# Kernel optimization log

Measured on AMD Instinct MI355X. Metric: run time of the kernel, lower is better.

## Reference

```python
import jax, jax.numpy as jnp
import numpy as np

N_NODES = 100000
N_EDGES = 3200000
BATCH = 16
HIDDEN = 64


def setup_inputs() -> dict:
    key = jax.random.key(0)
    k_mu, k_ei, k_w1, k_b1, k_w2, k_b2 = jax.random.split(key, 6)
    mu = jax.random.normal(k_mu, (BATCH, N_NODES), dtype=jnp.float32)
    edge_index = jax.random.randint(k_ei, (2, N_EDGES), 0, N_NODES, dtype=jnp.int64)
    # MLP params: Linear(1, hidden) -> GELU -> Linear(hidden, 1)
    W1 = jax.random.normal(k_w1, (1, HIDDEN), dtype=jnp.float32) * (1.0 / np.sqrt(1))
    b1 = jax.random.normal(k_b1, (HIDDEN,), dtype=jnp.float32) * 0.02
    W2 = jax.random.normal(k_w2, (HIDDEN, 1), dtype=jnp.float32) * (1.0 / np.sqrt(HIDDEN))
    b2 = jax.random.normal(k_b2, (1,), dtype=jnp.float32) * 0.02
    return {"mu": mu, "edge_index": edge_index, "W1": W1, "b1": b1, "W2": W2, "b2": b2}


def reference(mu, edge_index, W1, b1, W2, b2):
    row, col = edge_index[0], edge_index[1]
    B, N = mu.shape
    # degree of each destination node (clamped at 1)
    deg = jax.ops.segment_sum(jnp.ones_like(row, dtype=mu.dtype), row, num_segments=N)
    deg = jnp.maximum(deg, 1.0)  # [N]
    # batched message aggregation: gather source values, scatter-add to rows
    msgs = mu[:, col].T                                    # [E, B]
    agg = jax.ops.segment_sum(msgs, row, num_segments=N)   # [N, B]
    out = agg.T / deg[None, :]                             # [B, N]
    # tiny MLP applied per scalar: 1 -> hidden -> 1 with exact (erf) GELU
    h = jax.nn.gelu(out[..., None] * W1[0][None, None, :] + b1, approximate=False)  # [B, N, H]
    y = jnp.einsum('bnh,h->bn', h, W2[:, 0]) + b2[0]       # [B, N]
    return y
```

## Files before the change

### kernel.cpp

```cpp
#include <hip/hip_runtime.h>
#include <hip/hip_fp16.h>

#define N_NODES 100000
#define N_EDGES 3200000
#define BATCH   16
#define HIDDEN  64

#define NBINS   512
#define NPB     196
#define NSH     8
#define CAP_SH  1024
#define CAP_BIN 8192
#define EPB     8192
#define MAXW    16

#define PBLKS   391
#define TBLKS   196
#define LBLKS   17

#define LUT_SIZE  8192
#define LUT_LO    (-16.0f)
#define LUT_SCALE (LUT_SIZE / 32.0f)

typedef int v4i __attribute__((ext_vector_type(4)));

__global__ __launch_bounds__(512) void fused_part_prep_kernel(
    const int* __restrict__ ei, unsigned int* __restrict__ gcnt,
    unsigned int* __restrict__ packed,
    const float* __restrict__ mu, __half* __restrict__ mu_h,
    const float* __restrict__ W1, const float* __restrict__ b1,
    const float* __restrict__ W2, const float* __restrict__ b2,
    float* __restrict__ lut) {
  __shared__ int aux[NBINS];
  __shared__ int wsum[8];
  __shared__ unsigned int stag[EPB];
  __shared__ unsigned short sbin[EPB];

  int blk = blockIdx.x;
  int t = threadIdx.x;

  if (blk >= PBLKS) {
    if (blk < PBLKS + TBLKS) {
      int n = (blk - PBLKS) * 512 + t;
      if (n >= N_NODES) return;
      float4 o[4];
#pragma unroll
      for (int q = 0; q < 4; ++q) {
        o[q].x = mu[(q * 4 + 0) * N_NODES + n];
        o[q].y = mu[(q * 4 + 1) * N_NODES + n];
        o[q].z = mu[(q * 4 + 2) * N_NODES + n];
        o[q].w = mu[(q * 4 + 3) * N_NODES + n];
      }
      __half2 hh[8];
#pragma unroll
      for (int q = 0; q < 4; ++q) {
        hh[2 * q]     = __floats2half2_rn(o[q].x, o[q].y);
        hh[2 * q + 1] = __floats2half2_rn(o[q].z, o[q].w);
      }
      int4 w0 = make_int4(*(int*)&hh[0], *(int*)&hh[1], *(int*)&hh[2], *(int*)&hh[3]);
      int4 w1 = make_int4(*(int*)&hh[4], *(int*)&hh[5], *(int*)&hh[6], *(int*)&hh[7]);
      int4* dst = (int4*)(mu_h + (size_t)n * BATCH);
      dst[0] = w0;
      dst[1] = w1;
    } else {
      int i = (blk - PBLKS - TBLKS) * 512 + t;
      if (i > LUT_SIZE) return;
      float x = LUT_LO + (float)i / LUT_SCALE;
      float acc = b2[0];
      for (int h = 0; h < HIDDEN; ++h) {
        float z = fmaf(x, W1[h], b1[h]);
        float g = 0.5f * z * (1.0f + erff(z * 0.70710678118654752f));
        acc = fmaf(g, W2[h], acc);
      }
      lut[i] = acc;
    }
    return;
  }

  int base = blk * EPB;
  int nvalid = min(EPB, N_EDGES - base);
  int sh = blk & (NSH - 1);
  aux[t] = 0;
  __syncthreads();

  unsigned int pk[16];
  int bn[16];
  int rk[16];
  if (t * 16 + 16 <= nvalid) {
    const v4i* rp = (const v4i*)(ei + base + t * 16);
    const v4i* cp = (const v4i*)(ei + N_EDGES + base + t * 16);
    v4i rr[4], cc[4];
#pragma unroll
    for (int q = 0; q < 4; ++q) {
      rr[q] = rp[q];
      cc[q] = cp[q];
    }
#pragma unroll
    for (int q = 0; q < 4; ++q) {
#pragma unroll
      for (int u = 0; u < 4; ++u) {
        int k = q * 4 + u;
        int r = rr[q][u];
        int c = cc[q][u];
        int b = r / NPB;
        int rl = r - b * NPB;
        pk[k] = ((unsigned int)rl << 17) | (unsigned int)c;
        bn[k] = b;
      }
    }
#pragma unroll
    for (int k = 0; k < 16; ++k) rk[k] = atomicAdd(&aux[bn[k]], 1);
  } else {
#pragma unroll
    for (int k = 0; k < 16; ++k) {
      int e = t * 16 + k;
      if (e < nvalid) {
        int r = ei[base + e];
        int c = ei[N_EDGES + base + e];
        int b = r / NPB;
        int rl = r - b * NPB;
        pk[k] = ((unsigned int)rl << 17) | (unsigned int)c;
        bn[k] = b;
        rk[k] = atomicAdd(&aux[b], 1);
      } else {
        bn[k] = -1;
      }
    }
  }
  __syncthreads();

  int lane = t & 63;
  int wid = t >> 6;
  int v = aux[t];

  unsigned int gb = v ? atomicAdd(&gcnt[t * NSH + sh], (unsigned int)v) : 0u;

  int sv = v;
#pragma unroll
  for (int d = 1; d < 64; d <<= 1) {
    int n = __shfl_up(sv, d, 64);
    if (lane >= d) sv += n;
  }
  if (lane == 63) wsum[wid] = sv;
  __syncthreads();
  if (t < 8) {
    int s = wsum[t];
#pragma unroll
    for (int d = 1; d < 8; d <<= 1) {
      int n = __shfl_up(s, d, 8);
      if (t >= d) s += n;
    }
    wsum[t] = s;
  }
  __syncthreads();
  int pexcl = sv + (wid ? wsum[wid - 1] : 0) - v;
  aux[t] = pexcl;
  __syncthreads();

#pragma unroll
  for (int k = 0; k < 16; ++k) {
    if (bn[k] >= 0) {
      int p = aux[bn[k]] + rk[k];
      stag[p] = pk[k];
      sbin[p] = (unsigned short)bn[k];
    }
  }
  __syncthreads();

  aux[t] = (int)(sh * CAP_SH + gb) - pexcl;
  __syncthreads();

  unsigned int lim = (unsigned int)((sh + 1) * CAP_SH);
  for (int i = t; i < nvalid; i += 512) {
    int b = sbin[i];
    unsigned int pos = (unsigned int)(i + aux[b]);
    if (pos < lim)
      packed[(size_t)b * CAP_BIN + pos] = stag[i];
  }
}

__global__ __launch_bounds__(512) void scatter_apply_kernel(
    const unsigned int* __restrict__ gcnt, const unsigned int* __restrict__ packed,
    const __half* __restrict__ mu_h, const float* __restrict__ lut,
    float* __restrict__ out) {
  __shared__ unsigned int scol[CAP_BIN];
  __shared__ int dcnt[NPB];
  __shared__ int ebase[NPB];
  __shared__ int wpart[4];
  __shared__ int scnt_s[NSH];

  int t = threadIdx.x;
  int bin = blockIdx.x;

  const unsigned int* pp = packed + (size_t)bin * CAP_BIN;

  if (t < NPB) dcnt[t] = 0;
  if (t < NSH) scnt_s[t] = min((int)gcnt[bin * NSH + t], CAP_SH);
  __syncthreads();

  unsigned int w[MAXW];
  {
    const uint4* pp4 = (const uint4*)pp;
#pragma unroll
    for (int q = 0; q < 4; ++q) {
      uint4 a = pp4[t * 4 + q];
      w[q * 4 + 0] = a.x;
      w[q * 4 + 1] = a.y;
      w[q * 4 + 2] = a.z;
      w[q * 4 + 3] = a.w;
    }
  }

  int rk[MAXW];
#pragma unroll
  for (int k = 0; k < MAXW; ++k) {
    int i = t * 16 + k;
    int off = i & (CAP_SH - 1);
    rk[k] = (off < scnt_s[i >> 10]) ? atomicAdd(&dcnt[w[k] >> 17], 1) : 0;
  }
  __syncthreads();

  int v = 0, sv = 0;
  if (t < 256) {
    v = (t < NPB) ? dcnt[t] : 0;
    int lane = t & 63;
    sv = v;
#pragma unroll
    for (int d = 1; d < 64; d <<= 1) {
      int n = __shfl_up(sv, d, 64);
      if (lane >= d) sv += n;
    }
    if (lane == 63) wpart[t >> 6] = sv;
  }
  __syncthreads();
  if (t < 256) {
    int wid = t >> 6;
    int off = 0;
#pragma unroll
    for (int q = 0; q < 3; ++q)
      if (wid > q) off += wpart[q];
    if (t < NPB) ebase[t] = sv + off - v;
  }
  __syncthreads();

#pragma unroll
  for (int k = 0; k < MAXW; ++k) {
    int i = t * 16 + k;
    int off = i & (CAP_SH - 1);
    if (off < scnt_s[i >> 10]) {
      int rl = (int)(w[k] >> 17);
      scol[ebase[rl] + rk[k]] = w[k] & 0x1FFFFu;
    }
  }
  __syncthreads();

  const __half2* mu2 = (const __half2*)mu_h;
  int j2 = t & 7;
  int nsl = t >> 3;
  int binBase = bin * NPB;

#pragma unroll
  for (int pass = 0; pass < 4; ++pass) {
    int nl = pass * 64 + nsl;
    if (nl < NPB) {
      int node = binBase + nl;
      if (node < N_NODES) {
        int s = ebase[nl];
        int e = s + dcnt[nl];
        float2 a0 = {0.f, 0.f}, a1 = {0.f, 0.f};
        float2 a2 = {0.f, 0.f}, a3 = {0.f, 0.f};
        int i = s;
        for (; i + 8 <= e; i += 8) {
          int c0 = (int)scol[i];
          int c1 = (int)scol[i + 1];
          int c2 = (int)scol[i + 2];
          int c3 = (int)scol[i + 3];
          int c4 = (int)scol[i + 4];
          int c5 = (int)scol[i + 5];
          int c6 = (int)scol[i + 6];
          int c7 = (int)scol[i + 7];
          __half2 v0 = mu2[(size_t)c0 * 8 + j2];
          __half2 v1 = mu2[(size_t)c1 * 8 + j2];
          __half2 v2 = mu2[(size_t)c2 * 8 + j2];
          __half2 v3 = mu2[(size_t)c3 * 8 + j2];
          __half2 v4 = mu2[(size_t)c4 * 8 + j2];
          __half2 v5 = mu2[(size_t)c5 * 8 + j2];
          __half2 v6 = mu2[(size_t)c6 * 8 + j2];
          __half2 v7 = mu2[(size_t)c7 * 8 + j2];
          float2 f0 = __half22float2(v0);
          float2 f1 = __half22float2(v1);
          float2 f2 = __half22float2(v2);
          float2 f3 = __half22float2(v3);
          float2 f4 = __half22float2(v4);
          float2 f5 = __half22float2(v5);
          float2 f6 = __half22float2(v6);
          float2 f7 = __half22float2(v7);
          a0.x += f0.x + f4.x; a0.y += f0.y + f4.y;
          a1.x += f1.x + f5.x; a1.y += f1.y + f5.y;
          a2.x += f2.x + f6.x; a2.y += f2.y + f6.y;
          a3.x += f3.x + f7.x; a3.y += f3.y + f7.y;
        }
        for (; i + 4 <= e; i += 4) {
          int c0 = (int)scol[i];
          int c1 = (int)scol[i + 1];
          int c2 = (int)scol[i + 2];
          int c3 = (int)scol[i + 3];
          __half2 v0 = mu2[(size_t)c0 * 8 + j2];
          __half2 v1 = mu2[(size_t)c1 * 8 + j2];
          __half2 v2 = mu2[(size_t)c2 * 8 + j2];
          __half2 v3 = mu2[(size_t)c3 * 8 + j2];
          float2 f0 = __half22float2(v0);
          float2 f1 = __half22float2(v1);
          float2 f2 = __half22float2(v2);
          float2 f3 = __half22float2(v3);
          a0.x += f0.x; a0.y += f0.y;
          a1.x += f1.x; a1.y += f1.y;
          a2.x += f2.x; a2.y += f2.y;
          a3.x += f3.x; a3.y += f3.y;
        }
        for (; i < e; ++i) {
          float2 f = __half22float2(mu2[(size_t)scol[i] * 8 + j2]);
          a0.x += f.x; a0.y += f.y;
        }
        float sx = (a0.x + a1.x) + (a2.x + a3.x);
        float sy = (a0.y + a1.y) + (a2.y + a3.y);
        float dinv = 1.0f / (float)max(e - s, 1);

        float xs[2] = {sx * dinv, sy * dinv};
#pragma unroll
        for (int q = 0; q < 2; ++q) {
          float u = (xs[q] - LUT_LO) * LUT_SCALE;
          u = fminf(fmaxf(u, 0.0f), (float)LUT_SIZE - 0.001f);
          int ii = (int)u;
          float frac = u - (float)ii;
          float lo = lut[ii];
          float hi = lut[ii + 1];
          __builtin_nontemporal_store(fmaf(hi - lo, frac, lo),
                                      &out[(size_t)(2 * j2 + q) * N_NODES + node]);
        }
      }
    }
  }
}

extern "C" void kernel_launch(void* const* d_in, const int* in_sizes, int n_in,
                              void* d_out, int out_size, void* d_ws, size_t ws_size,
                              hipStream_t stream) {
  const float* mu = (const float*)d_in[0];
  const int*   ei = (const int*)d_in[1];
  const float* W1 = (const float*)d_in[2];
  const float* b1 = (const float*)d_in[3];
  const float* W2 = (const float*)d_in[4];
  const float* b2 = (const float*)d_in[5];
  float* out = (float*)d_out;

  __half* mu_h = (__half*)d_ws;
  float* lut  = (float*)(mu_h + (size_t)N_NODES * BATCH);
  unsigned int* gcnt = (unsigned int*)(lut + LUT_SIZE + 1);
  unsigned int* packed = gcnt + NBINS * NSH;

  (void)hipMemsetAsync(gcnt, 0, NBINS * NSH * sizeof(unsigned int), stream);

  fused_part_prep_kernel<<<PBLKS + TBLKS + LBLKS, 512, 0, stream>>>(
      ei, gcnt, packed, mu, mu_h, W1, b1, W2, b2, lut);

  scatter_apply_kernel<<<NBINS, 512, 0, stream>>>(gcnt, packed, mu_h, lut, out);
}
```

Baseline: 125.3 us.

## Write partitioned edges directly to global bins, drop LDS staging and scan

The partition kernel no longer sorts each block's edges by bin in shared memory before writing. It now writes every packed edge straight to its global bin slot, using the atomic rank and the global shard offset. This removes the block-wide prefix scan, two barriers and about 48KB of shared staging, which should raise occupancy. The shard count is doubled and shard capacity halved, and the scatter kernel's index shift is updated to match. The trade-off is that global stores are now less coalesced, and the smaller per-shard cap raises the risk of dropped edges when bins overflow.

```diff
diff --git a/kernel.cpp b/kernel.cpp
--- a/kernel.cpp
+++ b/kernel.cpp
@@ -8,8 +8,9 @@
 
 #define NBINS   512
 #define NPB     196
-#define NSH     8
-#define CAP_SH  1024
+#define NSH     16
+#define CAP_SH  512
+#define LOG_CAP_SH 9
 #define CAP_BIN 8192
 #define EPB     8192
 #define MAXW    16
@@ -32,9 +33,6 @@
     const float* __restrict__ W2, const float* __restrict__ b2,
     float* __restrict__ lut) {
   __shared__ int aux[NBINS];
-  __shared__ int wsum[8];
-  __shared__ unsigned int stag[EPB];
-  __shared__ unsigned short sbin[EPB];
 
   int blk = blockIdx.x;
   int t = threadIdx.x;
@@ -129,53 +127,19 @@
   }
   __syncthreads();
 
-  int lane = t & 63;
-  int wid = t >> 6;
   int v = aux[t];
-
   unsigned int gb = v ? atomicAdd(&gcnt[t * NSH + sh], (unsigned int)v) : 0u;
-
-  int sv = v;
-#pragma unroll
-  for (int d = 1; d < 64; d <<= 1) {
-    int n = __shfl_up(sv, d, 64);
-    if (lane >= d) sv += n;
-  }
-  if (lane == 63) wsum[wid] = sv;
-  __syncthreads();
-  if (t < 8) {
-    int s = wsum[t];
-#pragma unroll
-    for (int d = 1; d < 8; d <<= 1) {
-      int n = __shfl_up(s, d, 8);
-      if (t >= d) s += n;
-    }
-    wsum[t] = s;
-  }
-  __syncthreads();
-  int pexcl = sv + (wid ? wsum[wid - 1] : 0) - v;
-  aux[t] = pexcl;
-  __syncthreads();
-
+  aux[t] = (int)((unsigned int)(sh * CAP_SH) + gb);
+  __syncthreads();
+
+  unsigned int lim = (unsigned int)((sh + 1) * CAP_SH);
 #pragma unroll
   for (int k = 0; k < 16; ++k) {
     if (bn[k] >= 0) {
-      int p = aux[bn[k]] + rk[k];
-      stag[p] = pk[k];
-      sbin[p] = (unsigned short)bn[k];
-    }
-  }
-  __syncthreads();
-
-  aux[t] = (int)(sh * CAP_SH + gb) - pexcl;
-  __syncthreads();
-
-  unsigned int lim = (unsigned int)((sh + 1) * CAP_SH);
-  for (int i = t; i < nvalid; i += 512) {
-    int b = sbin[i];
-    unsigned int pos = (unsigned int)(i + aux[b]);
-    if (pos < lim)
-      packed[(size_t)b * CAP_BIN + pos] = stag[i];
+      unsigned int pos = (unsigned int)aux[bn[k]] + (unsigned int)rk[k];
+      if (pos < lim)
+        packed[(size_t)bn[k] * CAP_BIN + pos] = pk[k];
+    }
   }
 }
 
@@ -216,7 +180,7 @@
   for (int k = 0; k < MAXW; ++k) {
     int i = t * 16 + k;
     int off = i & (CAP_SH - 1);
-    rk[k] = (off < scnt_s[i >> 10]) ? atomicAdd(&dcnt[w[k] >> 17], 1) : 0;
+    rk[k] = (off < scnt_s[i >> LOG_CAP_SH]) ? atomicAdd(&dcnt[w[k] >> 17], 1) : 0;
   }
   __syncthreads();
 
@@ -247,7 +211,7 @@
   for (int k = 0; k < MAXW; ++k) {
     int i = t * 16 + k;
     int off = i & (CAP_SH - 1);
-    if (off < scnt_s[i >> 10]) {
+    if (off < scnt_s[i >> LOG_CAP_SH]) {
       int rl = (int)(w[k] >> 17);
       scol[ebase[rl] + rk[k]] = w[k] & 0x1FFFFu;
     }
```

Result: slower. 136.1 us (+8.6%).
